# Kernel optimization log

Measured on AMD Instinct MI355X. Metric: run time of the kernel, lower is better.

Reference implementation:

```python
import jax, jax.numpy as jnp
import numpy as np

I = 512   # input_size
H = 512   # hidden_size
Z = 0.1   # zoneout rate (eval-mode deterministic blend)
S = 128   # number of segments
B = 64    # batch


def setup_inputs() -> dict:
    rng = np.random.default_rng(0)
    durs = rng.integers(4, 13, size=(S, B)).astype(np.int64)  # [S, B], all >= 1
    T = int(durs.sum(0).max())
    key = jax.random.key(0)
    k0, k1, k2, k3, k4 = jax.random.split(key, 5)
    k = 1.0 / np.sqrt(H)
    x = jax.random.normal(k0, (T, B, I), jnp.float32)
    W_ih = jax.random.uniform(k1, (4 * H, I), jnp.float32, -k, k)
    W_hh = jax.random.uniform(k2, (4 * H, H), jnp.float32, -k, k)
    b_ih = jax.random.uniform(k3, (4 * H,), jnp.float32, -k, k)
    b_hh = jax.random.uniform(k4, (4 * H,), jnp.float32, -k, k)
    return {"x": x, "durs": jnp.asarray(durs), "W_ih": W_ih, "W_hh": W_hh,
            "b_ih": b_ih, "b_hh": b_hh}


def _duration_masks(durs, T):
    # durs: [S, B] -> per-batch segment-end (reset) frame indices and masks
    durs_bs = durs.T                                   # [B, S]
    reset_idx = jnp.cumsum(durs_bs, axis=1) - 1        # [B, S] last frame of each segment
    mel_lengths = jnp.sum(durs_bs, axis=1)             # [B]
    t = jnp.arange(T)
    reset_mask = jnp.any(t[None, :, None] == reset_idx[:, None, :], axis=-1)  # [B, T]
    valid = t[None, :] < mel_lengths[:, None]          # [B, T] frames within mel length
    retain = (~reset_mask) & valid                     # state kept where not reset/pad
    return reset_idx, retain.T, valid.T                # retain/valid as [T, B]


def reference(x, durs, W_ih, W_hh, b_ih, b_hh):
    T, Bb, _ = x.shape
    reset_idx, retain, valid = _duration_masks(durs, T)
    # Precompute the input contribution to the gates for all timesteps (one big GEMM)
    xg = jnp.einsum('tbi,gi->tbg', x, W_ih) + b_ih + b_hh   # [T, B, 4H]
    retain_f = retain.astype(x.dtype)                       # [T, B]

    def step(carry, inp):
        h, c = carry
        xg_t, retain_t = inp
        gates = xg_t + h @ W_hh.T                           # [B, 4H]
        i, f, g, o = jnp.split(gates, 4, axis=-1)           # torch LSTMCell order i,f,g,o
        i = jax.nn.sigmoid(i); f = jax.nn.sigmoid(f); o = jax.nn.sigmoid(o)
        g = jnp.tanh(g)
        c_new = f * c + i * g
        h_new = o * jnp.tanh(c_new)
        # eval-mode zoneout: deterministic blend with previous state
        h_z = Z * h + (1.0 - Z) * h_new
        c_z = Z * c + (1.0 - Z) * c_new
        m = retain_t[:, None]                               # zero state at segment resets / padding
        return (h_z * m, c_z * m), h_z

    h0 = jnp.zeros((Bb, H), x.dtype)
    (h, c), outputs = jax.lax.scan(step, (h0, h0), (xg, retain_f))
    outputs = outputs * valid[:, :, None].astype(outputs.dtype)  # [T, B, H]
    # segout: hidden state at each segment's last frame -> [B, S, H]
    segout = jnp.take_along_axis(outputs.transpose(1, 0, 2), reset_idx[:, :, None], axis=1)
    return outputs, h, c, segout
```

## Files before the change

kernel.cpp:

```cpp
#include <hip/hip_runtime.h>
#include <hip/hip_fp16.h>

#define IDIM 512
#define HDIM 512
#define NGATE 2048
#define SEGS 128
#define BATCH 64
#define ZK 0.1f

typedef _Float16 f16;
typedef _Float16 f16x8 __attribute__((ext_vector_type(8)));
typedef float f32x4 __attribute__((ext_vector_type(4)));

__device__ __forceinline__ void gload16(const void* g, void* l) {
  __builtin_amdgcn_global_load_lds((const __attribute__((address_space(1))) void*)g,
                                   (__attribute__((address_space(3))) void*)l, 16, 0, 0);
}
__device__ __forceinline__ float sigmoidf_(float x) { return 1.0f / (1.0f + __expf(-x)); }
__device__ __forceinline__ float tanhf_(float x) { return 2.0f / (1.0f + __expf(-2.0f * x)) - 1.0f; }

__global__ void prep_kernel(const int* __restrict__ durs, int4* __restrict__ meta,
                            int* __restrict__ Mk, int* __restrict__ mel) {
  __shared__ int hist[16];
  __shared__ int cur[16];
  int tid = threadIdx.x;
  if (tid < 16) hist[tid] = 0;
  __syncthreads();
  int b = tid;
  for (int s = 0; s < SEGS; ++s) {
    int d = durs[s * BATCH + b] & 15;
    atomicAdd(&hist[d], 1);
  }
  __syncthreads();
  if (tid == 0) {
    int run = 0;
    for (int d = 15; d >= 0; --d) { cur[d] = run; run += hist[d]; }
    for (int kk = 0; kk < 12; ++kk) Mk[kk] = cur[kk];
  }
  __syncthreads();
  int run = 0;
  for (int s = 0; s < SEGS; ++s) {
    int d = durs[s * BATCH + b] & 15;
    int pos = atomicAdd(&cur[d], 1);
    meta[pos] = make_int4(run, b, s, d);
    run += d;
  }
  mel[b] = run;
}

__global__ void wprep_kernel(const float* __restrict__ Wih, const float* __restrict__ Whh,
                             const float* __restrict__ bih, const float* __restrict__ bhh,
                             f16* __restrict__ Wc, float* __restrict__ biasp) {
  int n = blockIdx.x;
  int G = n >> 6, q = (n >> 4) & 3, r = n & 15;
  int j = G * 16 + r;
  int orig = q * 512 + j;
  for (int kk = threadIdx.x; kk < 1024; kk += blockDim.x) {
    float v = (kk < 512) ? Wih[(size_t)orig * 512 + kk] : Whh[(size_t)orig * 512 + kk - 512];
    Wc[(size_t)n * 1024 + kk] = (f16)v;
  }
  if (threadIdx.x == 0) biasp[n] = bih[orig] + bhh[orig];
}

__global__ void xconv_kernel(const float* __restrict__ x, f16* __restrict__ xh, long n8) {
  long i = (long)blockIdx.x * blockDim.x + threadIdx.x;
  long stride = (long)gridDim.x * blockDim.x;
  for (; i < n8; i += stride) {
    const float4* p = (const float4*)(x + i * 8);
    float4 a = p[0], bv = p[1];
    f16x8 o;
    o[0] = (f16)a.x;  o[1] = (f16)a.y;  o[2] = (f16)a.z;  o[3] = (f16)a.w;
    o[4] = (f16)bv.x; o[5] = (f16)bv.y; o[6] = (f16)bv.z; o[7] = (f16)bv.w;
    *(f16x8*)(xh + i * 8) = o;
  }
}

__global__ void zero_kernel(float* __restrict__ out, const int* __restrict__ mel, int T) {
  int bid = blockIdx.x;
  int tb = T * BATCH;
  if (bid < tb) {
    int t = bid / BATCH, b = bid - t * BATCH;
    if (t < mel[b]) return;
    float4* p = (float4*)(out + (size_t)bid * HDIM);
    p[threadIdx.x] = make_float4(0.f, 0.f, 0.f, 0.f);
  } else {
    int e = bid - tb;
    float4* p = (float4*)(out + (size_t)tb * HDIM + (size_t)e * HDIM);
    p[threadIdx.x] = make_float4(0.f, 0.f, 0.f, 0.f);
  }
}

template <bool FIRST>
__global__ void step_kernel(const f16* __restrict__ xh, const f16* __restrict__ Wc,
                            const float* __restrict__ biasp,
                            const f16* __restrict__ hprev, f16* __restrict__ hnext,
                            float* __restrict__ cst,
                            const int4* __restrict__ meta, const int* __restrict__ Mk,
                            float* __restrict__ out, int T, int k) {
  const int mk = Mk[k];
  const int m0 = blockIdx.y * 128;
  if (m0 >= mk) return;
  const int n0 = blockIdx.x * 128;

  __shared__ __align__(16) f16 At[128][64];
  __shared__ __align__(16) f16 Bt[128][64];
  __shared__ int4 metaS[128];

  const int tid = threadIdx.x;
  const int lane = tid & 63;
  const int w = tid >> 6;
  const int wr = w >> 1, wc = w & 1;

  if (tid < 128) metaS[tid] = meta[m0 + tid];

  const f16* xsrc[4];
  const f16* hsrc[4];
  const f16* wsrc[4];
#pragma unroll
  for (int i = 0; i < 4; ++i) {
    int r = m0 + w * 32 + i * 8 + (lane >> 3);
    int ra = (r < mk) ? r : 0;
    int4 mt = meta[ra];
    xsrc[i] = xh + ((size_t)(mt.x + k) * BATCH + mt.y) * IDIM;
    hsrc[i] = hprev + (size_t)ra * HDIM;
    wsrc[i] = Wc + (size_t)(n0 + w * 32 + i * 8 + (lane >> 3)) * 1024;
  }
  const int koff = (lane & 7) * 8;

  f32x4 acc[4][4];
#pragma unroll
  for (int a = 0; a < 4; ++a)
#pragma unroll
    for (int bb = 0; bb < 4; ++bb) acc[a][bb] = (f32x4){0.f, 0.f, 0.f, 0.f};

  const int KB = FIRST ? 8 : 16;
  for (int kb = 0; kb < KB; ++kb) {
    __syncthreads();
#pragma unroll
    for (int i = 0; i < 4; ++i) {
      const f16* s;
      if (FIRST) s = xsrc[i] + kb * 64 + koff;
      else       s = (kb < 8) ? (xsrc[i] + kb * 64 + koff) : (hsrc[i] + (kb - 8) * 64 + koff);
      gload16(s, &At[w * 32 + i * 8][0]);
    }
#pragma unroll
    for (int i = 0; i < 4; ++i) gload16(wsrc[i] + kb * 64 + koff, &Bt[w * 32 + i * 8][0]);
    __syncthreads();

    const int lr = lane & 15;
    const int lk = (lane >> 4) * 8;
#pragma unroll
    for (int ks = 0; ks < 2; ++ks) {
      f16x8 af[4], bfr[4];
#pragma unroll
      for (int f = 0; f < 4; ++f) af[f] = *(const f16x8*)&At[wr * 64 + f * 16 + lr][ks * 32 + lk];
#pragma unroll
      for (int f = 0; f < 4; ++f) bfr[f] = *(const f16x8*)&Bt[wc * 64 + f * 16 + lr][ks * 32 + lk];
#pragma unroll
      for (int fm = 0; fm < 4; ++fm)
#pragma unroll
        for (int fn = 0; fn < 4; ++fn)
          acc[fm][fn] = __builtin_amdgcn_mfma_f32_16x16x32_f16(af[fm], bfr[fn], acc[fm][fn], 0, 0, 0);
    }
  }

  const int r15 = lane & 15;
  float bq[4];
#pragma unroll
  for (int q = 0; q < 4; ++q) bq[q] = biasp[n0 + wc * 64 + q * 16 + r15];
  const int j = ((n0 + wc * 64) >> 6) * 16 + r15;
  const size_t segoff = (size_t)T * BATCH * HDIM + (size_t)2 * BATCH * HDIM;

#pragma unroll
  for (int fm = 0; fm < 4; ++fm) {
#pragma unroll
    for (int reg = 0; reg < 4; ++reg) {
      int m = m0 + wr * 64 + fm * 16 + ((lane >> 4) << 2) + reg;
      if (m >= mk) continue;
      int4 mt = metaS[m - m0];
      float gi = acc[fm][0][reg] + bq[0];
      float gf = acc[fm][1][reg] + bq[1];
      float gg = acc[fm][2][reg] + bq[2];
      float go = acc[fm][3][reg] + bq[3];
      float iv = sigmoidf_(gi), fv = sigmoidf_(gf);
      float gv = tanhf_(gg), ov = sigmoidf_(go);
      float cp, hp;
      if (FIRST) { cp = 0.f; hp = 0.f; }
      else {
        cp = cst[(size_t)m * HDIM + j];
        hp = (float)hprev[(size_t)m * HDIM + j];
      }
      float cn = fv * cp + iv * gv;
      float hn = ov * tanhf_(cn);
      float hz = ZK * hp + (1.f - ZK) * hn;
      float cz = ZK * cp + (1.f - ZK) * cn;
      out[((size_t)(mt.x + k) * BATCH + mt.y) * HDIM + j] = hz;
      if (k == mt.w - 1) {
        out[segoff + ((size_t)mt.y * SEGS + mt.z) * HDIM + j] = hz;
      } else {
        hnext[(size_t)m * HDIM + j] = (f16)hz;
        cst[(size_t)m * HDIM + j] = cz;
      }
    }
  }
}

extern "C" void kernel_launch(void* const* d_in, const int* in_sizes, int n_in,
                              void* d_out, int out_size, void* d_ws, size_t ws_size,
                              hipStream_t stream) {
  const float* x = (const float*)d_in[0];
  const int* durs = (const int*)d_in[1];
  const float* Wih = (const float*)d_in[2];
  const float* Whh = (const float*)d_in[3];
  const float* bih = (const float*)d_in[4];
  const float* bhh = (const float*)d_in[5];
  float* out = (float*)d_out;
  const int T = in_sizes[0] / (BATCH * IDIM);

  char* ws = (char*)d_ws;
  size_t off = 0;
  auto alloc = [&](size_t bytes) {
    void* p = ws + off;
    off = (off + bytes + 255) & ~(size_t)255;
    return p;
  };
  f16* xh     = (f16*)alloc((size_t)T * BATCH * IDIM * 2);
  f16* Wc     = (f16*)alloc((size_t)NGATE * 1024 * 2);
  float* biasp= (float*)alloc((size_t)NGATE * 4);
  f16* hst0   = (f16*)alloc((size_t)SEGS * BATCH * HDIM * 2);
  f16* hst1   = (f16*)alloc((size_t)SEGS * BATCH * HDIM * 2);
  float* cst  = (float*)alloc((size_t)SEGS * BATCH * HDIM * 4);
  int4* meta  = (int4*)alloc((size_t)SEGS * BATCH * 16);
  int* Mk     = (int*)alloc(64);
  int* mel    = (int*)alloc(64);

  prep_kernel<<<1, 64, 0, stream>>>(durs, meta, Mk, mel);
  wprep_kernel<<<NGATE, 256, 0, stream>>>(Wih, Whh, bih, bhh, Wc, biasp);
  long n8 = (long)T * BATCH * IDIM / 8;
  xconv_kernel<<<2048, 256, 0, stream>>>(x, xh, n8);
  zero_kernel<<<T * BATCH + 128, 128, 0, stream>>>(out, mel, T);

  dim3 sgrid(16, 64);
  step_kernel<true><<<sgrid, 256, 0, stream>>>(xh, Wc, biasp, hst0, hst1, cst, meta, Mk, out, T, 0);
  for (int k = 1; k < 12; ++k) {
    f16* hp = (k & 1) ? hst1 : hst0;
    f16* hn = (k & 1) ? hst0 : hst1;
    step_kernel<false><<<sgrid, 256, 0, stream>>>(xh, Wc, biasp, hp, hn, cst, meta, Mk, out, T, k);
  }
}
```

Before: 657.0 us.

## Add double-buffered 256x256 tile step kernel for early timesteps

Adds a 256x256 tile variant of the per-timestep LSTM gate GEMM with 512 threads. It double-buffers LDS with the global-to-LDS loads interleaved between MFMA phases, uses an XOR swizzle to avoid LDS bank conflicts, remaps workgroups with an XCD-aware swizzle, and raises s_setprio around the MFMA blocks. This variant handles steps 0-7, where many segment rows are still active, while the original 128-tile kernel stays for steps 8-11. The goal is more data reuse and less load latency on the large early GEMMs. The cost is fewer workgroups, lower occupancy, and more wasted tiles when the active row count is not a multiple of 256.

```diff
diff --git a/kernel.cpp b/kernel.cpp
--- a/kernel.cpp
+++ b/kernel.cpp
@@ -87,6 +87,203 @@
     int e = bid - tb;
     float4* p = (float4*)(out + (size_t)tb * HDIM + (size_t)e * HDIM);
     p[threadIdx.x] = make_float4(0.f, 0.f, 0.f, 0.f);
+  }
+}
+
+template <bool FIRST>
+__global__ __launch_bounds__(512, 1)
+void step256_kernel(const f16* __restrict__ xh, const f16* __restrict__ Wc,
+                    const float* __restrict__ biasp,
+                    const f16* __restrict__ hprev, f16* __restrict__ hnext,
+                    float* __restrict__ cst,
+                    const int4* __restrict__ meta, const int* __restrict__ Mk,
+                    float* __restrict__ out, int T, int k) {
+  const int mk = Mk[k];
+  const int nbx = gridDim.x;
+  const int nwg = nbx * gridDim.y;
+  const int orig = blockIdx.y * nbx + blockIdx.x;
+  const int cpx = nwg >> 3;
+  const int swz = (orig & 7) * cpx + (orig >> 3);
+  const int by = swz / nbx, bx = swz - by * nbx;
+  const int m0 = by * 256;
+  if (m0 >= mk) return;
+  const int n0 = bx * 256;
+
+  __shared__ __align__(16) f16 As[2][256][64];
+  __shared__ __align__(16) f16 Bs[2][256][64];
+  __shared__ int4 metaS[256];
+
+  const int tid = threadIdx.x;
+  const int lane = tid & 63;
+  const int w = tid >> 6;
+  const int wr = w >> 2;
+  const int wc = w & 3;
+  const int lr = lane & 15;
+  const int lk = lane >> 4;
+
+  if (tid < 256) metaS[tid] = meta[m0 + tid];
+
+  const int swzc = (((lane & 7) ^ ((lane >> 3) & 7)) << 3);
+  size_t xoff[4];
+  int ra4[4];
+#pragma unroll
+  for (int o = 0; o < 4; ++o) {
+    int trow = o * 64 + w * 8 + (lane >> 3);
+    int r = m0 + trow;
+    int ra = (r < mk) ? r : 0;
+    int4 mt = meta[ra];
+    xoff[o] = ((size_t)(mt.x + k) * BATCH + mt.y) * IDIM + swzc;
+    ra4[o] = ra;
+  }
+
+  auto stageA = [&](int o, int kb, int slot) {
+    const f16* src;
+    if (FIRST || kb < 8) src = xh + xoff[o] + kb * 64;
+    else src = hprev + (size_t)ra4[o] * HDIM + (kb - 8) * 64 + swzc;
+    gload16(src, &As[slot][o * 64 + w * 8][0]);
+  };
+  auto stageB = [&](int o, int kb, int slot) {
+    int trow = o * 64 + w * 8 + (lane >> 3);
+    gload16(Wc + (size_t)(n0 + trow) * 1024 + (size_t)kb * 64 + swzc,
+            &Bs[slot][o * 64 + w * 8][0]);
+  };
+  auto stageOp = [&](int idx, int kb, int slot) {
+    if (idx < 4) stageA(idx, kb, slot);
+    else stageB(idx - 4, kb, slot);
+  };
+
+  auto lda = [&](int slot, int h, int f, int ks) -> f16x8 {
+    int row = wr * 128 + h * 64 + f * 16 + lr;
+    int ch = (((ks * 4 + lk) ^ (lr & 7)) << 3);
+    return *(const f16x8*)&As[slot][row][ch];
+  };
+  auto ldb = [&](int slot, int q, int ks) -> f16x8 {
+    int row = wc * 64 + q * 16 + lr;
+    int ch = (((ks * 4 + lk) ^ (lr & 7)) << 3);
+    return *(const f16x8*)&Bs[slot][row][ch];
+  };
+
+  f32x4 acc[8][4];
+#pragma unroll
+  for (int a = 0; a < 8; ++a)
+#pragma unroll
+    for (int bb = 0; bb < 4; ++bb) acc[a][bb] = (f32x4){0.f, 0.f, 0.f, 0.f};
+
+#pragma unroll
+  for (int idx = 0; idx < 8; ++idx) stageOp(idx, 0, 0);
+  asm volatile("s_waitcnt vmcnt(0)" ::: "memory");
+  __builtin_amdgcn_s_barrier();
+
+  const int KB = FIRST ? 8 : 16;
+  f16x8 aF[4][2], bF[4][2];
+
+  for (int kt = 0; kt < KB; ++kt) {
+    const int s = kt & 1;
+    const int sn = s ^ 1;
+    const int kn = kt + 1;
+    const bool st = (kn < KB);
+
+#pragma unroll
+    for (int f = 0; f < 4; ++f)
+#pragma unroll
+      for (int ks = 0; ks < 2; ++ks) aF[f][ks] = lda(s, 0, f, ks);
+#pragma unroll
+    for (int q = 0; q < 4; ++q)
+#pragma unroll
+      for (int ks = 0; ks < 2; ++ks) bF[q][ks] = ldb(s, q, ks);
+    if (st) { stageOp(0, kn, sn); stageOp(1, kn, sn); stageOp(2, kn, sn); }
+    __builtin_amdgcn_s_barrier();
+    __builtin_amdgcn_s_setprio(1);
+#pragma unroll
+    for (int f = 0; f < 4; ++f)
+#pragma unroll
+      for (int fn = 0; fn < 2; ++fn)
+#pragma unroll
+        for (int ks = 0; ks < 2; ++ks)
+          acc[f][fn] = __builtin_amdgcn_mfma_f32_16x16x32_f16(aF[f][ks], bF[fn][ks], acc[f][fn], 0, 0, 0);
+    __builtin_amdgcn_s_setprio(0);
+    __builtin_amdgcn_s_barrier();
+
+    if (st) { stageOp(3, kn, sn); stageOp(4, kn, sn); stageOp(5, kn, sn); }
+    __builtin_amdgcn_s_barrier();
+    __builtin_amdgcn_s_setprio(1);
+#pragma unroll
+    for (int f = 0; f < 4; ++f)
+#pragma unroll
+      for (int fn = 2; fn < 4; ++fn)
+#pragma unroll
+        for (int ks = 0; ks < 2; ++ks)
+          acc[f][fn] = __builtin_amdgcn_mfma_f32_16x16x32_f16(aF[f][ks], bF[fn][ks], acc[f][fn], 0, 0, 0);
+    __builtin_amdgcn_s_setprio(0);
+    __builtin_amdgcn_s_barrier();
+
+#pragma unroll
+    for (int f = 0; f < 4; ++f)
+#pragma unroll
+      for (int ks = 0; ks < 2; ++ks) aF[f][ks] = lda(s, 1, f, ks);
+    if (st) { stageOp(6, kn, sn); stageOp(7, kn, sn); }
+    __builtin_amdgcn_s_barrier();
+    __builtin_amdgcn_s_setprio(1);
+#pragma unroll
+    for (int f = 0; f < 4; ++f)
+#pragma unroll
+      for (int fn = 0; fn < 2; ++fn)
+#pragma unroll
+        for (int ks = 0; ks < 2; ++ks)
+          acc[4 + f][fn] = __builtin_amdgcn_mfma_f32_16x16x32_f16(aF[f][ks], bF[fn][ks], acc[4 + f][fn], 0, 0, 0);
+    __builtin_amdgcn_s_setprio(0);
+    __builtin_amdgcn_s_barrier();
+
+    __builtin_amdgcn_s_setprio(1);
+#pragma unroll
+    for (int f = 0; f < 4; ++f)
+#pragma unroll
+      for (int fn = 2; fn < 4; ++fn)
+#pragma unroll
+        for (int ks = 0; ks < 2; ++ks)
+          acc[4 + f][fn] = __builtin_amdgcn_mfma_f32_16x16x32_f16(aF[f][ks], bF[fn][ks], acc[4 + f][fn], 0, 0, 0);
+    __builtin_amdgcn_s_setprio(0);
+    asm volatile("s_waitcnt vmcnt(0)" ::: "memory");
+    __builtin_amdgcn_s_barrier();
+  }
+
+  float bq[4];
+#pragma unroll
+  for (int q = 0; q < 4; ++q) bq[q] = biasp[n0 + wc * 64 + q * 16 + lr];
+  const int j = ((n0 + wc * 64) >> 6) * 16 + lr;
+  const size_t segoff = (size_t)T * BATCH * HDIM + (size_t)2 * BATCH * HDIM;
+
+#pragma unroll
+  for (int fm = 0; fm < 8; ++fm) {
+#pragma unroll
+    for (int reg = 0; reg < 4; ++reg) {
+      int m = m0 + wr * 128 + fm * 16 + ((lane >> 4) << 2) + reg;
+      if (m >= mk) continue;
+      int4 mt = metaS[m - m0];
+      float gi = acc[fm][0][reg] + bq[0];
+      float gf = acc[fm][1][reg] + bq[1];
+      float gg = acc[fm][2][reg] + bq[2];
+      float go = acc[fm][3][reg] + bq[3];
+      float iv = sigmoidf_(gi), fv = sigmoidf_(gf);
+      float gv = tanhf_(gg), ov = sigmoidf_(go);
+      float cp, hp;
+      if (FIRST) { cp = 0.f; hp = 0.f; }
+      else {
+        cp = cst[(size_t)m * HDIM + j];
+        hp = (float)hprev[(size_t)m * HDIM + j];
+      }
+      float cn = fv * cp + iv * gv;
+      float hn = ov * tanhf_(cn);
+      float hz = ZK * hp + (1.f - ZK) * hn;
+      float cz = ZK * cp + (1.f - ZK) * cn;
+      out[((size_t)(mt.x + k) * BATCH + mt.y) * HDIM + j] = hz;
+      if (k == mt.w - 1) {
+        out[segoff + ((size_t)mt.y * SEGS + mt.z) * HDIM + j] = hz;
+      } else {
+        hnext[(size_t)m * HDIM + j] = (f16)hz;
+        cst[(size_t)m * HDIM + j] = cz;
+      }
+    }
   }
 }
 
@@ -240,9 +437,15 @@
   xconv_kernel<<<2048, 256, 0, stream>>>(x, xh, n8);
   zero_kernel<<<T * BATCH + 128, 128, 0, stream>>>(out, mel, T);
 
+  dim3 hgrid(8, 32);
+  step256_kernel<true><<<hgrid, 512, 0, stream>>>(xh, Wc, biasp, hst0, hst1, cst, meta, Mk, out, T, 0);
+  for (int k = 1; k < 8; ++k) {
+    f16* hp = (k & 1) ? hst1 : hst0;
+    f16* hn = (k & 1) ? hst0 : hst1;
+    step256_kernel<false><<<hgrid, 512, 0, stream>>>(xh, Wc, biasp, hp, hn, cst, meta, Mk, out, T, k);
+  }
   dim3 sgrid(16, 64);
-  step_kernel<true><<<sgrid, 256, 0, stream>>>(xh, Wc, biasp, hst0, hst1, cst, meta, Mk, out, T, 0);
-  for (int k = 1; k < 12; ++k) {
+  for (int k = 8; k < 12; ++k) {
     f16* hp = (k & 1) ? hst1 : hst0;
     f16* hn = (k & 1) ? hst0 : hst1;
     step_kernel<false><<<sgrid, 256, 0, stream>>>(xh, Wc, biasp, hp, hn, cst, meta, Mk, out, T, k);
```

Measured after the change: 650.1 us. About the same (-1.0%).

## Overlap next-step input GEMM with current recurrent step in fused kernel

Applied to the files above, without the earlier changes.

Splits the per-step GEMM so each launch computes only the h·W_hh part for step k, while a second half of the grid computes the x·W_ih projection for step k+1 into a double-buffered fp16 gate buffer. This roughly halves the serial critical-path K per step and gives extra concurrent blocks to fill the GPU. The cost is an extra launch, fp16 rounding of the precomputed input gates, and extra global traffic to write and read the gate buffers. The zero kernel is also changed to a grid-stride loop with a fixed grid.

```diff
diff --git a/kernel.cpp b/kernel.cpp
--- a/kernel.cpp
+++ b/kernel.cpp
@@ -27,10 +27,7 @@
   if (tid < 16) hist[tid] = 0;
   __syncthreads();
   int b = tid;
-  for (int s = 0; s < SEGS; ++s) {
-    int d = durs[s * BATCH + b] & 15;
-    atomicAdd(&hist[d], 1);
-  }
+  for (int s = 0; s < SEGS; ++s) atomicAdd(&hist[durs[s * BATCH + b] & 15], 1);
   __syncthreads();
   if (tid == 0) {
     int run = 0;
@@ -50,14 +47,14 @@
 
 __global__ void wprep_kernel(const float* __restrict__ Wih, const float* __restrict__ Whh,
                              const float* __restrict__ bih, const float* __restrict__ bhh,
-                             f16* __restrict__ Wc, float* __restrict__ biasp) {
+                             f16* __restrict__ Wihp, f16* __restrict__ Whhp,
+                             float* __restrict__ biasp) {
   int n = blockIdx.x;
   int G = n >> 6, q = (n >> 4) & 3, r = n & 15;
-  int j = G * 16 + r;
-  int orig = q * 512 + j;
-  for (int kk = threadIdx.x; kk < 1024; kk += blockDim.x) {
-    float v = (kk < 512) ? Wih[(size_t)orig * 512 + kk] : Whh[(size_t)orig * 512 + kk - 512];
-    Wc[(size_t)n * 1024 + kk] = (f16)v;
+  int orig = q * 512 + G * 16 + r;
+  for (int kk = threadIdx.x; kk < 512; kk += blockDim.x) {
+    Wihp[(size_t)n * 512 + kk] = (f16)Wih[(size_t)orig * 512 + kk];
+    Whhp[(size_t)n * 512 + kk] = (f16)Whh[(size_t)orig * 512 + kk];
   }
   if (threadIdx.x == 0) biasp[n] = bih[orig] + bhh[orig];
 }
@@ -75,57 +72,45 @@
   }
 }
 
-__global__ void zero_kernel(float* __restrict__ out, const int* __restrict__ mel, int T) {
-  int bid = blockIdx.x;
+__global__ void zero_kernel(float* __restrict__ out, const int* __restrict__ mel,
+                            int T, int total) {
   int tb = T * BATCH;
-  if (bid < tb) {
-    int t = bid / BATCH, b = bid - t * BATCH;
-    if (t < mel[b]) return;
-    float4* p = (float4*)(out + (size_t)bid * HDIM);
-    p[threadIdx.x] = make_float4(0.f, 0.f, 0.f, 0.f);
-  } else {
-    int e = bid - tb;
-    float4* p = (float4*)(out + (size_t)tb * HDIM + (size_t)e * HDIM);
-    p[threadIdx.x] = make_float4(0.f, 0.f, 0.f, 0.f);
-  }
-}
-
-template <bool FIRST>
-__global__ void step_kernel(const f16* __restrict__ xh, const f16* __restrict__ Wc,
-                            const float* __restrict__ biasp,
-                            const f16* __restrict__ hprev, f16* __restrict__ hnext,
-                            float* __restrict__ cst,
-                            const int4* __restrict__ meta, const int* __restrict__ Mk,
-                            float* __restrict__ out, int T, int k) {
-  const int mk = Mk[k];
-  const int m0 = blockIdx.y * 128;
-  if (m0 >= mk) return;
-  const int n0 = blockIdx.x * 128;
-
-  __shared__ __align__(16) f16 At[128][64];
-  __shared__ __align__(16) f16 Bt[128][64];
+  for (int bid = blockIdx.x; bid < total; bid += gridDim.x) {
+    if (bid < tb) {
+      int t = bid / BATCH, b = bid - t * BATCH;
+      if (t < mel[b]) continue;
+      float4* p = (float4*)(out + (size_t)bid * HDIM);
+      p[threadIdx.x] = make_float4(0.f, 0.f, 0.f, 0.f);
+    } else {
+      int e = bid - tb;
+      float4* p = (float4*)(out + (size_t)tb * HDIM + (size_t)e * HDIM);
+      p[threadIdx.x] = make_float4(0.f, 0.f, 0.f, 0.f);
+    }
+  }
+}
+
+__global__ __launch_bounds__(256)
+void step_fused(const f16* __restrict__ xh, const f16* __restrict__ Whhp,
+                const f16* __restrict__ Wihp, const float* __restrict__ biasp,
+                const f16* __restrict__ xg_cur, f16* __restrict__ xg_next,
+                const f16* __restrict__ hprev, f16* __restrict__ hnext,
+                float* __restrict__ cst,
+                const int4* __restrict__ meta, const int* __restrict__ Mk,
+                float* __restrict__ out, int T, int k) {
+  __shared__ __align__(16) f16 SMEM[16384];
+  f16 (*At)[64] = (f16(*)[64])SMEM;
+  f16 (*Bt)[64] = (f16(*)[64])(SMEM + 8192);
   __shared__ int4 metaS[128];
 
   const int tid = threadIdx.x;
   const int lane = tid & 63;
   const int w = tid >> 6;
   const int wr = w >> 1, wc = w & 1;
-
-  if (tid < 128) metaS[tid] = meta[m0 + tid];
-
-  const f16* xsrc[4];
-  const f16* hsrc[4];
-  const f16* wsrc[4];
-#pragma unroll
-  for (int i = 0; i < 4; ++i) {
-    int r = m0 + w * 32 + i * 8 + (lane >> 3);
-    int ra = (r < mk) ? r : 0;
-    int4 mt = meta[ra];
-    xsrc[i] = xh + ((size_t)(mt.x + k) * BATCH + mt.y) * IDIM;
-    hsrc[i] = hprev + (size_t)ra * HDIM;
-    wsrc[i] = Wc + (size_t)(n0 + w * 32 + i * 8 + (lane >> 3)) * 1024;
-  }
+  const int lrr = lane & 15;
+  const int lkk = (lane >> 4) * 8;
+  const int lk4 = (lane >> 4) << 2;
   const int koff = (lane & 7) * 8;
+  const int n0 = blockIdx.x * 128;
 
   f32x4 acc[4][4];
 #pragma unroll
@@ -133,74 +118,146 @@
 #pragma unroll
     for (int bb = 0; bb < 4; ++bb) acc[a][bb] = (f32x4){0.f, 0.f, 0.f, 0.f};
 
-  const int KB = FIRST ? 8 : 16;
-  for (int kb = 0; kb < KB; ++kb) {
+  if (blockIdx.y < 64) {
+    if (k < 0) return;
+    const int mk = Mk[k];
+    const int m0 = blockIdx.y * 128;
+    if (m0 >= mk) return;
+
+    if (tid < 128) metaS[tid] = meta[m0 + tid];
+
+    if (k > 0) {
+      const f16* hsrc[4];
+      const f16* wsrc[4];
+#pragma unroll
+      for (int i = 0; i < 4; ++i) {
+        int r = m0 + w * 32 + i * 8 + (lane >> 3);
+        int ra = (r < mk) ? r : 0;
+        hsrc[i] = hprev + (size_t)ra * HDIM;
+        wsrc[i] = Whhp + (size_t)(n0 + w * 32 + i * 8 + (lane >> 3)) * 512;
+      }
+      for (int kb = 0; kb < 8; ++kb) {
+        __syncthreads();
+#pragma unroll
+        for (int i = 0; i < 4; ++i) gload16(hsrc[i] + kb * 64 + koff, &At[w * 32 + i * 8][0]);
+#pragma unroll
+        for (int i = 0; i < 4; ++i) gload16(wsrc[i] + kb * 64 + koff, &Bt[w * 32 + i * 8][0]);
+        __syncthreads();
+#pragma unroll
+        for (int ks = 0; ks < 2; ++ks) {
+          f16x8 af[4], bfr[4];
+#pragma unroll
+          for (int f = 0; f < 4; ++f) af[f] = *(const f16x8*)&At[wr * 64 + f * 16 + lrr][ks * 32 + lkk];
+#pragma unroll
+          for (int f = 0; f < 4; ++f) bfr[f] = *(const f16x8*)&Bt[wc * 64 + f * 16 + lrr][ks * 32 + lkk];
+#pragma unroll
+          for (int fm = 0; fm < 4; ++fm)
+#pragma unroll
+            for (int fn = 0; fn < 4; ++fn)
+              acc[fm][fn] = __builtin_amdgcn_mfma_f32_16x16x32_f16(af[fm], bfr[fn], acc[fm][fn], 0, 0, 0);
+        }
+      }
+    } else {
+      __syncthreads();
+    }
+
+    float bq[4];
+#pragma unroll
+    for (int q = 0; q < 4; ++q) bq[q] = biasp[n0 + wc * 64 + q * 16 + lrr];
+    const int nb = n0 + wc * 64 + lrr;
+    const int j = ((n0 + wc * 64) >> 6) * 16 + lrr;
+    const size_t segoff = (size_t)T * BATCH * HDIM + (size_t)2 * BATCH * HDIM;
+
+#pragma unroll
+    for (int fm = 0; fm < 4; ++fm) {
+#pragma unroll
+      for (int reg = 0; reg < 4; ++reg) {
+        int m = m0 + wr * 64 + fm * 16 + lk4 + reg;
+        if (m >= mk) continue;
+        int4 mt = metaS[m - m0];
+        const f16* xgp = xg_cur + (size_t)m * NGATE;
+        float gi = acc[fm][0][reg] + (float)xgp[nb] + bq[0];
+        float gf = acc[fm][1][reg] + (float)xgp[nb + 16] + bq[1];
+        float gg = acc[fm][2][reg] + (float)xgp[nb + 32] + bq[2];
+        float go = acc[fm][3][reg] + (float)xgp[nb + 48] + bq[3];
+        float iv = sigmoidf_(gi), fv = sigmoidf_(gf);
+        float gv = tanhf_(gg), ov = sigmoidf_(go);
+        float cp, hp;
+        if (k == 0) { cp = 0.f; hp = 0.f; }
+        else {
+          cp = cst[(size_t)m * HDIM + j];
+          hp = (float)hprev[(size_t)m * HDIM + j];
+        }
+        float cn = fv * cp + iv * gv;
+        float hn = ov * tanhf_(cn);
+        float hz = ZK * hp + (1.f - ZK) * hn;
+        float cz = ZK * cp + (1.f - ZK) * cn;
+        out[((size_t)(mt.x + k) * BATCH + mt.y) * HDIM + j] = hz;
+        if (k == mt.w - 1) {
+          out[segoff + ((size_t)mt.y * SEGS + mt.z) * HDIM + j] = hz;
+        } else {
+          hnext[(size_t)m * HDIM + j] = (f16)hz;
+          cst[(size_t)m * HDIM + j] = cz;
+        }
+      }
+    }
+  } else {
+    const int kt = k + 1;
+    if (kt >= 12) return;
+    const int mk = Mk[kt];
+    const int m0 = (blockIdx.y - 64) * 128;
+    if (m0 >= mk) return;
+
+    const f16* xsrc[4];
+    const f16* wsrc[4];
+#pragma unroll
+    for (int i = 0; i < 4; ++i) {
+      int r = m0 + w * 32 + i * 8 + (lane >> 3);
+      int ra = (r < mk) ? r : 0;
+      int4 mt = meta[ra];
+      xsrc[i] = xh + ((size_t)(mt.x + kt) * BATCH + mt.y) * IDIM;
+      wsrc[i] = Wihp + (size_t)(n0 + w * 32 + i * 8 + (lane >> 3)) * 512;
+    }
+    for (int kb = 0; kb < 8; ++kb) {
+      __syncthreads();
+#pragma unroll
+      for (int i = 0; i < 4; ++i) gload16(xsrc[i] + kb * 64 + koff, &At[w * 32 + i * 8][0]);
+#pragma unroll
+      for (int i = 0; i < 4; ++i) gload16(wsrc[i] + kb * 64 + koff, &Bt[w * 32 + i * 8][0]);
+      __syncthreads();
+#pragma unroll
+      for (int ks = 0; ks < 2; ++ks) {
+        f16x8 af[4], bfr[4];
+#pragma unroll
+        for (int f = 0; f < 4; ++f) af[f] = *(const f16x8*)&At[wr * 64 + f * 16 + lrr][ks * 32 + lkk];
+#pragma unroll
+        for (int f = 0; f < 4; ++f) bfr[f] = *(const f16x8*)&Bt[wc * 64 + f * 16 + lrr][ks * 32 + lkk];
+#pragma unroll
+        for (int fm = 0; fm < 4; ++fm)
+#pragma unroll
+          for (int fn = 0; fn < 4; ++fn)
+            acc[fm][fn] = __builtin_amdgcn_mfma_f32_16x16x32_f16(af[fm], bfr[fn], acc[fm][fn], 0, 0, 0);
+      }
+    }
+
     __syncthreads();
-#pragma unroll
-    for (int i = 0; i < 4; ++i) {
-      const f16* s;
-      if (FIRST) s = xsrc[i] + kb * 64 + koff;
-      else       s = (kb < 8) ? (xsrc[i] + kb * 64 + koff) : (hsrc[i] + (kb - 8) * 64 + koff);
-      gload16(s, &At[w * 32 + i * 8][0]);
-    }
-#pragma unroll
-    for (int i = 0; i < 4; ++i) gload16(wsrc[i] + kb * 64 + koff, &Bt[w * 32 + i * 8][0]);
+    f16* SM2 = SMEM;
+#pragma unroll
+    for (int fm = 0; fm < 4; ++fm)
+#pragma unroll
+      for (int reg = 0; reg < 4; ++reg) {
+        int lm = wr * 64 + fm * 16 + lk4 + reg;
+#pragma unroll
+        for (int q = 0; q < 4; ++q)
+          SM2[lm * 128 + wc * 64 + q * 16 + lrr] = (f16)acc[fm][q][reg];
+      }
     __syncthreads();
-
-    const int lr = lane & 15;
-    const int lk = (lane >> 4) * 8;
-#pragma unroll
-    for (int ks = 0; ks < 2; ++ks) {
-      f16x8 af[4], bfr[4];
-#pragma unroll
-      for (int f = 0; f < 4; ++f) af[f] = *(const f16x8*)&At[wr * 64 + f * 16 + lr][ks * 32 + lk];
-#pragma unroll
-      for (int f = 0; f < 4; ++f) bfr[f] = *(const f16x8*)&Bt[wc * 64 + f * 16 + lr][ks * 32 + lk];
-#pragma unroll
-      for (int fm = 0; fm < 4; ++fm)
-#pragma unroll
-        for (int fn = 0; fn < 4; ++fn)
-          acc[fm][fn] = __builtin_amdgcn_mfma_f32_16x16x32_f16(af[fm], bfr[fn], acc[fm][fn], 0, 0, 0);
-    }
-  }
-
-  const int r15 = lane & 15;
-  float bq[4];
-#pragma unroll
-  for (int q = 0; q < 4; ++q) bq[q] = biasp[n0 + wc * 64 + q * 16 + r15];
-  const int j = ((n0 + wc * 64) >> 6) * 16 + r15;
-  const size_t segoff = (size_t)T * BATCH * HDIM + (size_t)2 * BATCH * HDIM;
-
-#pragma unroll
-  for (int fm = 0; fm < 4; ++fm) {
-#pragma unroll
-    for (int reg = 0; reg < 4; ++reg) {
-      int m = m0 + wr * 64 + fm * 16 + ((lane >> 4) << 2) + reg;
-      if (m >= mk) continue;
-      int4 mt = metaS[m - m0];
-      float gi = acc[fm][0][reg] + bq[0];
-      float gf = acc[fm][1][reg] + bq[1];
-      float gg = acc[fm][2][reg] + bq[2];
-      float go = acc[fm][3][reg] + bq[3];
-      float iv = sigmoidf_(gi), fv = sigmoidf_(gf);
-      float gv = tanhf_(gg), ov = sigmoidf_(go);
-      float cp, hp;
-      if (FIRST) { cp = 0.f; hp = 0.f; }
-      else {
-        cp = cst[(size_t)m * HDIM + j];
-        hp = (float)hprev[(size_t)m * HDIM + j];
-      }
-      float cn = fv * cp + iv * gv;
-      float hn = ov * tanhf_(cn);
-      float hz = ZK * hp + (1.f - ZK) * hn;
-      float cz = ZK * cp + (1.f - ZK) * cn;
-      out[((size_t)(mt.x + k) * BATCH + mt.y) * HDIM + j] = hz;
-      if (k == mt.w - 1) {
-        out[segoff + ((size_t)mt.y * SEGS + mt.z) * HDIM + j] = hz;
-      } else {
-        hnext[(size_t)m * HDIM + j] = (f16)hz;
-        cst[(size_t)m * HDIM + j] = cz;
-      }
+#pragma unroll
+    for (int i = 0; i < 8; ++i) {
+      int idx = i * 256 + tid;
+      int lm = idx >> 4, c = idx & 15;
+      *(f16x8*)(xg_next + (size_t)(m0 + lm) * NGATE + n0 + c * 8) =
+          *(const f16x8*)&SM2[lm * 128 + c * 8];
     }
   }
 }
@@ -224,27 +281,34 @@
     off = (off + bytes + 255) & ~(size_t)255;
     return p;
   };
-  f16* xh     = (f16*)alloc((size_t)T * BATCH * IDIM * 2);
-  f16* Wc     = (f16*)alloc((size_t)NGATE * 1024 * 2);
-  float* biasp= (float*)alloc((size_t)NGATE * 4);
-  f16* hst0   = (f16*)alloc((size_t)SEGS * BATCH * HDIM * 2);
-  f16* hst1   = (f16*)alloc((size_t)SEGS * BATCH * HDIM * 2);
-  float* cst  = (float*)alloc((size_t)SEGS * BATCH * HDIM * 4);
-  int4* meta  = (int4*)alloc((size_t)SEGS * BATCH * 16);
-  int* Mk     = (int*)alloc(64);
-  int* mel    = (int*)alloc(64);
+  f16* xh      = (f16*)alloc((size_t)T * BATCH * IDIM * 2);
+  f16* Wihp    = (f16*)alloc((size_t)NGATE * 512 * 2);
+  f16* Whhp    = (f16*)alloc((size_t)NGATE * 512 * 2);
+  float* biasp = (float*)alloc((size_t)NGATE * 4);
+  f16* xg0     = (f16*)alloc((size_t)SEGS * BATCH * NGATE * 2);
+  f16* xg1     = (f16*)alloc((size_t)SEGS * BATCH * NGATE * 2);
+  f16* hst0    = (f16*)alloc((size_t)SEGS * BATCH * HDIM * 2);
+  f16* hst1    = (f16*)alloc((size_t)SEGS * BATCH * HDIM * 2);
+  float* cst   = (float*)alloc((size_t)SEGS * BATCH * HDIM * 4);
+  int4* meta   = (int4*)alloc((size_t)SEGS * BATCH * 16);
+  int* Mk      = (int*)alloc(64);
+  int* mel     = (int*)alloc(64);
 
   prep_kernel<<<1, 64, 0, stream>>>(durs, meta, Mk, mel);
-  wprep_kernel<<<NGATE, 256, 0, stream>>>(Wih, Whh, bih, bhh, Wc, biasp);
+  wprep_kernel<<<NGATE, 256, 0, stream>>>(Wih, Whh, bih, bhh, Wihp, Whhp, biasp);
   long n8 = (long)T * BATCH * IDIM / 8;
   xconv_kernel<<<2048, 256, 0, stream>>>(x, xh, n8);
-  zero_kernel<<<T * BATCH + 128, 128, 0, stream>>>(out, mel, T);
-
-  dim3 sgrid(16, 64);
-  step_kernel<true><<<sgrid, 256, 0, stream>>>(xh, Wc, biasp, hst0, hst1, cst, meta, Mk, out, T, 0);
-  for (int k = 1; k < 12; ++k) {
+  zero_kernel<<<2048, 128, 0, stream>>>(out, mel, T, T * BATCH + 128);
+
+  dim3 grid(16, 128);
+  step_fused<<<grid, 256, 0, stream>>>(xh, Whhp, Wihp, biasp, xg1, xg0,
+                                       hst0, hst1, cst, meta, Mk, out, T, -1);
+  for (int k = 0; k < 12; ++k) {
+    f16* xgc = (k & 1) ? xg1 : xg0;
+    f16* xgn = (k & 1) ? xg0 : xg1;
     f16* hp = (k & 1) ? hst1 : hst0;
     f16* hn = (k & 1) ? hst0 : hst1;
-    step_kernel<false><<<sgrid, 256, 0, stream>>>(xh, Wc, biasp, hp, hn, cst, meta, Mk, out, T, k);
-  }
-}
+    step_fused<<<grid, 256, 0, stream>>>(xh, Whhp, Wihp, biasp, xgc, xgn,
+                                         hp, hn, cst, meta, Mk, out, T, k);
+  }
+}
```

New measurement: 815.0 us. +24.1%, slower.
